# Performance work log

Measured on AMD Instinct MI355X. Metric: run time of the kernel, lower is better.

## Reference

```python
import jax, jax.numpy as jnp
import numpy as np
from jax import lax

B, T, N_OBS, N_ACT, H = 256, 4096, 64, 18, 8


def _linear_params(k, fan_out, fan_in):
    # torch nn.Linear default init: U(-1/sqrt(fan_in), 1/sqrt(fan_in))
    lim = 1.0 / np.sqrt(fan_in)
    kw, kb = jax.random.split(k)
    W = jax.random.uniform(kw, (fan_out, fan_in), minval=-lim, maxval=lim, dtype=jnp.float32)
    b = jax.random.uniform(kb, (fan_out,), minval=-lim, maxval=lim, dtype=jnp.float32)
    return W, b


def setup_inputs() -> dict:
    key = jax.random.key(0)
    ks = jax.random.split(key, 8)
    W1, b1 = _linear_params(ks[0], 4, N_OBS)          # linear1
    W2, b2 = _linear_params(ks[1], H, 4)              # linear2
    Wih, bih = _linear_params(ks[2], 4 * H, H)        # lstm input-hidden (i,f,g,o)
    Whh, bhh = _linear_params(ks[3], 4 * H, H)        # lstm hidden-hidden
    Wa, ba = _linear_params(ks[4], N_ACT, H)          # action_distribution
    Wv, bv = _linear_params(ks[5], 1, H)              # values
    states = jax.random.normal(ks[6], (B, T, N_OBS), dtype=jnp.float32)
    dones = jax.random.randint(ks[7], (B, T), 0, 2).astype(bool)
    hx = jnp.zeros((2, T, H), dtype=jnp.float32)
    return dict(states=states, dones=dones, hx=hx,
                W1=W1, b1=b1, W2=W2, b2=b2,
                Wih=Wih, bih=bih, Whh=Whh, bhh=bhh,
                Wa=Wa, ba=ba, Wv=Wv, bv=bv)


def reference(states, dones, hx, W1, b1, W2, b2, Wih, bih, Whh, bhh, Wa, ba, Wv, bv):
    b, t, _ = states.shape
    # MLP encoder on flattened [B*T, n_obs] (same math as original flatten)
    x = jax.nn.relu(jnp.einsum('btn,kn->btk', states, W1) + b1)   # [B,T,4]
    x = jax.nn.relu(jnp.einsum('btk,hk->bth', x, W2) + b2)        # [B,T,8]

    def step(carry, inp):
        h, c = carry                      # each [T,H] (lstm batch = trajectory_length)
        xt, dt = inp                      # [T,H], [T] bool
        mask = dt[:, None]                # done.view(1,-1,1) broadcast reset
        h = jnp.where(mask, 0.0, h)
        c = jnp.where(mask, 0.0, c)
        gates = xt @ Wih.T + bih + h @ Whh.T + bhh  # [T,4H]
        i, f, g, o = jnp.split(gates, 4, axis=-1)
        i = jax.nn.sigmoid(i)
        f = jax.nn.sigmoid(f)
        g = jnp.tanh(g)
        o = jax.nn.sigmoid(o)
        c2 = f * c + i * g
        h2 = o * jnp.tanh(c2)
        return (h2, c2), h2

    # sequential scan over the BATCH dim (faithful to the original unbind(dim=0) loop)
    _, lstm_out = lax.scan(step, (hx[0], hx[1]), (x, dones))      # [B,T,H]

    flat = lstm_out.reshape(b * t, -1)                            # cat(lstm_out, 0)
    actions = flat @ Wa.T + ba                                    # [B*T, n_actions]
    values = flat @ Wv.T + bv                                     # [B*T, 1]
    return actions.reshape(b, -1, t), values.reshape(b, t)
```

## Files before the change

kernel.cpp:

```cpp
#include <hip/hip_runtime.h>

#define T_DIM 4096
#define B_DIM 256
#define NSEG 8
#define SEGLEN 32
#define BSTRIDE ((size_t)T_DIM * 64)

#define SIGM(X)  __builtin_amdgcn_rcpf(1.f + __expf(-(X)))
#define TANH(X)  fmaf(2.f, __builtin_amdgcn_rcpf(1.f + __expf(-2.f * (X))), -1.f)


#define LOAD_WEIGHTS                                                           \
    float w1s[4][8];                                                           \
    _Pragma("unroll") for (int m = 0; m < 4; ++m)                              \
        _Pragma("unroll") for (int k = 0; k < 8; ++k)                          \
            w1s[m][k] = W1[m * 64 + j * 8 + k];                                \
    float b1r0 = b1[0], b1r1 = b1[1], b1r2 = b1[2], b1r3 = b1[3];              \
    float w2s0 = W2[j*4+0], w2s1 = W2[j*4+1], w2s2 = W2[j*4+2], w2s3 = W2[j*4+3]; \
    float b2r = b2[j];                                                         \
    float wI[8], wF[8], wG[8], wO[8], uI[8], uF[8], uG[8], uO[8];              \
    _Pragma("unroll") for (int k = 0; k < 8; ++k) {                            \
        wI[k] = Wih[j * 8 + k];        uI[k] = Whh[j * 8 + k];                 \
        wF[k] = Wih[(8 + j) * 8 + k];  uF[k] = Whh[(8 + j) * 8 + k];           \
        wG[k] = Wih[(16 + j) * 8 + k]; uG[k] = Whh[(16 + j) * 8 + k];          \
        wO[k] = Wih[(24 + j) * 8 + k]; uO[k] = Whh[(24 + j) * 8 + k];          \
    }                                                                          \
    float bI = bih[j] + bhh[j],      bF = bih[8 + j] + bhh[8 + j];             \
    float bG = bih[16 + j] + bhh[16 + j], bO = bih[24 + j] + bhh[24 + j];      \
    float hw0[8], hw1[8], hw2[8];                                              \
    float hb0 = ba[j], hb1 = ba[8 + j], hb2 = 0.f;                             \
    _Pragma("unroll") for (int k = 0; k < 8; ++k) {                            \
        hw0[k] = Wa[j * 8 + k]; hw1[k] = Wa[(8 + j) * 8 + k]; hw2[k] = 0.f;    \
    }                                                                          \
    if (j < 2) {                                                               \
        _Pragma("unroll") for (int k = 0; k < 8; ++k) hw2[k] = Wa[(16+j)*8+k]; \
        hb2 = ba[16 + j];                                                      \
    } else if (j == 2) {                                                       \
        _Pragma("unroll") for (int k = 0; k < 8; ++k) hw2[k] = Wv[k];          \
        hb2 = bv[0];                                                           \
    }

#define CORE_S(DONEE, SA, SV)                                                  \
        float p0 = SA.x * w1s[0][0], p1 = SA.x * w1s[1][0];                    \
        float p2 = SA.x * w1s[2][0], p3 = SA.x * w1s[3][0];                    \
        p0 = fmaf(SA.y, w1s[0][1], p0); p1 = fmaf(SA.y, w1s[1][1], p1);        \
        p2 = fmaf(SA.y, w1s[2][1], p2); p3 = fmaf(SA.y, w1s[3][1], p3);        \
        p0 = fmaf(SA.z, w1s[0][2], p0); p1 = fmaf(SA.z, w1s[1][2], p1);        \
        p2 = fmaf(SA.z, w1s[2][2], p2); p3 = fmaf(SA.z, w1s[3][2], p3);        \
        p0 = fmaf(SA.w, w1s[0][3], p0); p1 = fmaf(SA.w, w1s[1][3], p1);        \
        p2 = fmaf(SA.w, w1s[2][3], p2); p3 = fmaf(SA.w, w1s[3][3], p3);        \
        p0 = fmaf(SV.x, w1s[0][4], p0); p1 = fmaf(SV.x, w1s[1][4], p1);        \
        p2 = fmaf(SV.x, w1s[2][4], p2); p3 = fmaf(SV.x, w1s[3][4], p3);        \
        p0 = fmaf(SV.y, w1s[0][5], p0); p1 = fmaf(SV.y, w1s[1][5], p1);        \
        p2 = fmaf(SV.y, w1s[2][5], p2); p3 = fmaf(SV.y, w1s[3][5], p3);        \
        p0 = fmaf(SV.z, w1s[0][6], p0); p1 = fmaf(SV.z, w1s[1][6], p1);        \
        p2 = fmaf(SV.z, w1s[2][6], p2); p3 = fmaf(SV.z, w1s[3][6], p3);        \
        p0 = fmaf(SV.w, w1s[0][7], p0); p1 = fmaf(SV.w, w1s[1][7], p1);        \
        p2 = fmaf(SV.w, w1s[2][7], p2); p3 = fmaf(SV.w, w1s[3][7], p3);        \
        p0 += __shfl_xor(p0, 1, 64); p1 += __shfl_xor(p1, 1, 64);              \
        p2 += __shfl_xor(p2, 1, 64); p3 += __shfl_xor(p3, 1, 64);              \
        p0 += __shfl_xor(p0, 2, 64); p1 += __shfl_xor(p1, 2, 64);              \
        p2 += __shfl_xor(p2, 2, 64); p3 += __shfl_xor(p3, 2, 64);              \
        p0 += __shfl_xor(p0, 4, 64); p1 += __shfl_xor(p1, 4, 64);              \
        p2 += __shfl_xor(p2, 4, 64); p3 += __shfl_xor(p3, 4, 64);              \
        float y0 = fmaxf(p0 + b1r0, 0.f);                                      \
        float y1 = fmaxf(p1 + b1r1, 0.f);                                      \
        float y2 = fmaxf(p2 + b1r2, 0.f);                                      \
        float y3 = fmaxf(p3 + b1r3, 0.f);                                      \
        float xj = fmaf(y3, w2s3, fmaf(y2, w2s2, fmaf(y1, w2s1,                \
                   fmaf(y0, w2s0, b2r))));                                     \
        xj = fmaxf(xj, 0.f);                                                   \
        float x0 = __shfl(xj, gb | 0, 64);                                     \
        float x1 = __shfl(xj, gb | 1, 64);                                     \
        float xx2 = __shfl(xj, gb | 2, 64);                                    \
        float x3 = __shfl(xj, gb | 3, 64);                                     \
        float x4 = __shfl(xj, gb | 4, 64);                                     \
        float x5 = __shfl(xj, gb | 5, 64);                                     \
        float x6 = __shfl(xj, gb | 6, 64);                                     \
        float x7 = __shfl(xj, gb | 7, 64);                                     \
        float gi = bI, gf = bF, gg = bG, go = bO;                              \
        gi = fmaf(x0, wI[0], gi); gi = fmaf(x1, wI[1], gi);                    \
        gi = fmaf(xx2, wI[2], gi); gi = fmaf(x3, wI[3], gi);                   \
        gi = fmaf(x4, wI[4], gi); gi = fmaf(x5, wI[5], gi);                    \
        gi = fmaf(x6, wI[6], gi); gi = fmaf(x7, wI[7], gi);                    \
        gf = fmaf(x0, wF[0], gf); gf = fmaf(x1, wF[1], gf);                    \
        gf = fmaf(xx2, wF[2], gf); gf = fmaf(x3, wF[3], gf);                   \
        gf = fmaf(x4, wF[4], gf); gf = fmaf(x5, wF[5], gf);                    \
        gf = fmaf(x6, wF[6], gf); gf = fmaf(x7, wF[7], gf);                    \
        gg = fmaf(x0, wG[0], gg); gg = fmaf(x1, wG[1], gg);                    \
        gg = fmaf(xx2, wG[2], gg); gg = fmaf(x3, wG[3], gg);                   \
        gg = fmaf(x4, wG[4], gg); gg = fmaf(x5, wG[5], gg);                    \
        gg = fmaf(x6, wG[6], gg); gg = fmaf(x7, wG[7], gg);                    \
        go = fmaf(x0, wO[0], go); go = fmaf(x1, wO[1], go);                    \
        go = fmaf(xx2, wO[2], go); go = fmaf(x3, wO[3], go);                   \
        go = fmaf(x4, wO[4], go); go = fmaf(x5, wO[5], go);                    \
        go = fmaf(x6, wO[6], go); go = fmaf(x7, wO[7], go);                    \
        float dI = h[0] * uI[0], dF = h[0] * uF[0];                            \
        float dG = h[0] * uG[0], dO = h[0] * uO[0];                            \
        dI = fmaf(h[1], uI[1], dI); dF = fmaf(h[1], uF[1], dF);                \
        dG = fmaf(h[1], uG[1], dG); dO = fmaf(h[1], uO[1], dO);                \
        dI = fmaf(h[2], uI[2], dI); dF = fmaf(h[2], uF[2], dF);                \
        dG = fmaf(h[2], uG[2], dG); dO = fmaf(h[2], uO[2], dO);                \
        dI = fmaf(h[3], uI[3], dI); dF = fmaf(h[3], uF[3], dF);                \
        dG = fmaf(h[3], uG[3], dG); dO = fmaf(h[3], uO[3], dO);                \
        dI = fmaf(h[4], uI[4], dI); dF = fmaf(h[4], uF[4], dF);                \
        dG = fmaf(h[4], uG[4], dG); dO = fmaf(h[4], uO[4], dO);                \
        dI = fmaf(h[5], uI[5], dI); dF = fmaf(h[5], uF[5], dF);                \
        dG = fmaf(h[5], uG[5], dG); dO = fmaf(h[5], uO[5], dO);                \
        dI = fmaf(h[6], uI[6], dI); dF = fmaf(h[6], uF[6], dF);                \
        dG = fmaf(h[6], uG[6], dG); dO = fmaf(h[6], uO[6], dO);                \
        dI = fmaf(h[7], uI[7], dI); dF = fmaf(h[7], uF[7], dF);                \
        dG = fmaf(h[7], uG[7], dG); dO = fmaf(h[7], uO[7], dO);                \
        float GI = (DONEE) ? gi : (gi + dI);                                   \
        float GF = (DONEE) ? gf : (gf + dF);                                   \
        float GG = (DONEE) ? gg : (gg + dG);                                   \
        float GO = (DONEE) ? go : (go + dO);                                   \
        float cin = (DONEE) ? 0.f : c;                                         \
        float i_ = SIGM(GI);                                                   \
        float f_ = SIGM(GF);                                                   \
        float g_ = TANH(GG);                                                   \
        float o_ = SIGM(GO);                                                   \
        float c2 = fmaf(f_, cin, i_ * g_);                                     \
        float th = TANH(c2);                                                   \
        float h2 = o_ * th;

#define HEADS                                                                  \
        float o0 = hb0, o1 = hb1, o2 = hb2;                                    \
        o0 = fmaf(h[0], hw0[0], o0); o1 = fmaf(h[0], hw1[0], o1);              \
        o2 = fmaf(h[0], hw2[0], o2);                                           \
        o0 = fmaf(h[1], hw0[1], o0); o1 = fmaf(h[1], hw1[1], o1);              \
        o2 = fmaf(h[1], hw2[1], o2);                                           \
        o0 = fmaf(h[2], hw0[2], o0); o1 = fmaf(h[2], hw1[2], o1);              \
        o2 = fmaf(h[2], hw2[2], o2);                                           \
        o0 = fmaf(h[3], hw0[3], o0); o1 = fmaf(h[3], hw1[3], o1);              \
        o2 = fmaf(h[3], hw2[3], o2);                                           \
        o0 = fmaf(h[4], hw0[4], o0); o1 = fmaf(h[4], hw1[4], o1);              \
        o2 = fmaf(h[4], hw2[4], o2);                                           \
        o0 = fmaf(h[5], hw0[5], o0); o1 = fmaf(h[5], hw1[5], o1);              \
        o2 = fmaf(h[5], hw2[5], o2);                                           \
        o0 = fmaf(h[6], hw0[6], o0); o1 = fmaf(h[6], hw1[6], o1);              \
        o2 = fmaf(h[6], hw2[6], o2);                                           \
        o0 = fmaf(h[7], hw0[7], o0); o1 = fmaf(h[7], hw1[7], o1);              \
        o2 = fmaf(h[7], hw2[7], o2);

#define HSHFL                                                                  \
        h[0] = __shfl(h2, gb | 0, 64); h[1] = __shfl(h2, gb | 1, 64);          \
        h[2] = __shfl(h2, gb | 2, 64); h[3] = __shfl(h2, gb | 3, 64);          \
        h[4] = __shfl(h2, gb | 4, 64); h[5] = __shfl(h2, gb | 5, 64);          \
        h[6] = __shfl(h2, gb | 6, 64); h[7] = __shfl(h2, gb | 7, 64);

__global__ __launch_bounds__(64) void pass1_kernel(
    const float* __restrict__ states, const int* __restrict__ dones,
    const float* __restrict__ hx,
    const float* __restrict__ W1, const float* __restrict__ b1,
    const float* __restrict__ W2, const float* __restrict__ b2,
    const float* __restrict__ Wih, const float* __restrict__ bih,
    const float* __restrict__ Whh, const float* __restrict__ bhh,
    const float* __restrict__ Wa, const float* __restrict__ ba,
    const float* __restrict__ Wv, const float* __restrict__ bv,
    float* __restrict__ out,
    float* __restrict__ carryH, float* __restrict__ carryC,
    int* __restrict__ fdbuf)
{
    int lane = threadIdx.x;
    int col  = lane >> 3;
    int j    = lane & 7;
    int gb   = lane & 56;
    int s    = blockIdx.x >> 9;
    int tb   = blockIdx.x & 511;
    int t    = tb * 8 + col;
    int b0   = s * SEGLEN;

    LOAD_WEIGHTS

    float h[8]; float c;
    if (s == 0) {
#pragma unroll
        for (int m = 0; m < 8; ++m) h[m] = hx[t * 8 + m];
        c = hx[T_DIM * 8 + t * 8 + j];
    } else {
#pragma unroll
        for (int m = 0; m < 8; ++m) h[m] = 0.f;
        c = 0.f;
    }

    const float* sbase = states + ((size_t)b0 * T_DIM + t) * 64 + j * 8;
    const int*   dbase = dones + (size_t)b0 * T_DIM + t;
    float* outA = out + ((size_t)b0 * T_DIM + t) * 18;
    float* outV = out + (size_t)18 * B_DIM * T_DIM + (size_t)b0 * T_DIM + t;
    int fd = SEGLEN;

    int dn0, dn1, dn2, dn3;
    float4 sa0, sv0, sa1, sv1, sa2, sv2, sa3, sv3;
#define PF(I) \
    dn##I = dbase[(size_t)(I) * T_DIM]; \
    sa##I = *(const float4*)(sbase + (size_t)(I) * BSTRIDE); \
    sv##I = *(const float4*)(sbase + (size_t)(I) * BSTRIDE + 4);
    PF(0) PF(1) PF(2) PF(3)
#undef PF

#define P1STEP(KK, DN, SA, SV)                                                 \
    {                                                                          \
        int done = DN; float4 sa = SA, sv = SV;                                \
        int kp = (KK) + 4; kp = (kp > SEGLEN - 1) ? (SEGLEN - 1) : kp;         \
        DN = dbase[(size_t)kp * T_DIM];                                        \
        SA = *(const float4*)(sbase + (size_t)kp * BSTRIDE);                   \
        SV = *(const float4*)(sbase + (size_t)kp * BSTRIDE + 4);               \
        CORE_S(done, sa, sv)                                                   \
        c = c2;                                                                \
        HSHFL                                                                  \
        fd = (done && fd == SEGLEN) ? (KK) : fd;                               \
        HEADS                                                                  \
        outA[j] = o0; outA[8 + j] = o1;                                        \
        if (j < 2) outA[16 + j] = o2; else if (j == 2) *outV = o2;             \
        outA += (size_t)T_DIM * 18; outV += T_DIM;                             \
    }

    for (int k0 = 0; k0 < SEGLEN; k0 += 4) {
        P1STEP(k0 + 0, dn0, sa0, sv0);
        P1STEP(k0 + 1, dn1, sa1, sv1);
        P1STEP(k0 + 2, dn2, sa2, sv2);
        P1STEP(k0 + 3, dn3, sa3, sv3);
    }
#undef P1STEP

    carryH[((size_t)s * T_DIM + t) * 8 + j] = h[j];
    carryC[((size_t)s * T_DIM + t) * 8 + j] = c;
    if (j == 0) fdbuf[(size_t)s * T_DIM + t] = fd;
}

__global__ __launch_bounds__(64) void pass2_kernel(
    const float* __restrict__ states, const int* __restrict__ dones,
    const float* __restrict__ W1, const float* __restrict__ b1,
    const float* __restrict__ W2, const float* __restrict__ b2,
    const float* __restrict__ Wih, const float* __restrict__ bih,
    const float* __restrict__ Whh, const float* __restrict__ bhh,
    const float* __restrict__ Wa, const float* __restrict__ ba,
    const float* __restrict__ Wv, const float* __restrict__ bv,
    float* __restrict__ out,
    const float* __restrict__ carryH, const float* __restrict__ carryC,
    const int* __restrict__ fdbuf)
{
    int lane = threadIdx.x;
    int col  = lane >> 3;
    int j    = lane & 7;
    int gb   = lane & 56;
    int s    = 1 + (int)(blockIdx.x >> 9);
    int tb   = blockIdx.x & 511;
    int t    = tb * 8 + col;

    LOAD_WEIGHTS

    const float* sb2 = states + (size_t)t * 64 + j * 8;

    float h[8]; float c;
    bool prev_exact = (s == 1) ||
                      (fdbuf[(size_t)(s - 1) * T_DIM + t] < SEGLEN);
    if (__all(prev_exact)) {
#pragma unroll
        for (int m = 0; m < 8; ++m)
            h[m] = carryH[((size_t)(s - 1) * T_DIM + t) * 8 + m];
        c = carryC[((size_t)(s - 1) * T_DIM + t) * 8 + j];
    } else {
#pragma unroll
        for (int m = 0; m < 8; ++m) h[m] = carryH[(size_t)t * 8 + m];
        c = carryC[(size_t)t * 8 + j];
        for (int p = 1; p <= s - 1; ++p) {
            size_t bb = (size_t)p * SEGLEN;
            for (int k = 0; k < SEGLEN; ++k) {
                int done = dones[(bb + k) * T_DIM + t];
                float4 sa = *(const float4*)(sb2 + (bb + k) * BSTRIDE);
                float4 sv = *(const float4*)(sb2 + (bb + k) * BSTRIDE + 4);
                CORE_S(done, sa, sv)
                c = c2;
                HSHFL
            }
            int fdp = fdbuf[(size_t)p * T_DIM + t];
            if (fdp < SEGLEN) {
#pragma unroll
                for (int m = 0; m < 8; ++m)
                    h[m] = carryH[((size_t)p * T_DIM + t) * 8 + m];
                c = carryC[((size_t)p * T_DIM + t) * 8 + j];
            }
        }
    }

    int fd = fdbuf[(size_t)s * T_DIM + t];
    int wmax = fd;
#pragma unroll
    for (int d = 1; d < 64; d <<= 1) {
        int o = __shfl_xor(wmax, d, 64);
        wmax = (o > wmax) ? o : wmax;
    }
    size_t bbase = (size_t)s * SEGLEN;
    float4 csa = *(const float4*)(sb2 + bbase * BSTRIDE);
    float4 csv = *(const float4*)(sb2 + bbase * BSTRIDE + 4);
    for (int k = 0; k < wmax; ++k) {
        bool act = (k < fd);
        float4 sa = csa, sv = csv;
        int kn = k + 1; kn = (kn > SEGLEN - 1) ? (SEGLEN - 1) : kn;
        csa = *(const float4*)(sb2 + (bbase + kn) * BSTRIDE);
        csv = *(const float4*)(sb2 + (bbase + kn) * BSTRIDE + 4);
        CORE_S(0, sa, sv)
        c = act ? c2 : c;
        float n0 = __shfl(h2, gb | 0, 64), n1 = __shfl(h2, gb | 1, 64);
        float n2 = __shfl(h2, gb | 2, 64), n3 = __shfl(h2, gb | 3, 64);
        float n4 = __shfl(h2, gb | 4, 64), n5 = __shfl(h2, gb | 5, 64);
        float n6 = __shfl(h2, gb | 6, 64), n7 = __shfl(h2, gb | 7, 64);
        h[0] = act ? n0 : h[0]; h[1] = act ? n1 : h[1];
        h[2] = act ? n2 : h[2]; h[3] = act ? n3 : h[3];
        h[4] = act ? n4 : h[4]; h[5] = act ? n5 : h[5];
        h[6] = act ? n6 : h[6]; h[7] = act ? n7 : h[7];
        HEADS
        if (act) {
            float* outA = out + ((bbase + k) * T_DIM + t) * 18;
            outA[j] = o0; outA[8 + j] = o1;
            if (j < 2) outA[16 + j] = o2;
            else if (j == 2)
                out[(size_t)18 * B_DIM * T_DIM + (bbase + k) * T_DIM + t] = o2;
        }
    }
}

extern "C" void kernel_launch(void* const* d_in, const int* in_sizes, int n_in,
                              void* d_out, int out_size, void* d_ws, size_t ws_size,
                              hipStream_t stream) {
    (void)in_sizes; (void)n_in; (void)out_size; (void)ws_size;
    const float* states = (const float*)d_in[0];
    const int*   dones  = (const int*)d_in[1];
    const float* hx     = (const float*)d_in[2];
    const float* W1     = (const float*)d_in[3];
    const float* b1     = (const float*)d_in[4];
    const float* W2     = (const float*)d_in[5];
    const float* b2     = (const float*)d_in[6];
    const float* Wih    = (const float*)d_in[7];
    const float* bih    = (const float*)d_in[8];
    const float* Whh    = (const float*)d_in[9];
    const float* bhh    = (const float*)d_in[10];
    const float* Wa     = (const float*)d_in[11];
    const float* ba     = (const float*)d_in[12];
    const float* Wv     = (const float*)d_in[13];
    const float* bv     = (const float*)d_in[14];
    float* out = (float*)d_out;

    float* carryH = (float*)d_ws;
    float* carryC = (float*)((char*)d_ws + (1u << 20));
    int*   fdbuf  = (int*)((char*)d_ws + (2u << 20));

    pass1_kernel<<<NSEG * 512, 64, 0, stream>>>(states, dones, hx, W1, b1, W2, b2,
                                                Wih, bih, Whh, bhh, Wa, ba, Wv, bv,
                                                out, carryH, carryC, fdbuf);
    pass2_kernel<<<(NSEG - 1) * 512, 64, 0, stream>>>(states, dones, W1, b1, W2, b2,
                                                      Wih, bih, Whh, bhh, Wa, ba, Wv, bv,
                                                      out, carryH, carryC, fdbuf);
}
```

Baseline: 96.17 us.

## Replace lane shuffles with DPP xor-gathers and compute layer-2 redundantly per lane

The 8-lane hidden-state broadcast now uses an xor-permuted layout, built from DPP quad_perm moves for xor 1 and 2 and ds_bpermute only for xor 4. To match, the Whh, head and initial-state weights are reindexed by j^m. The first two reduction stages also switch to DPP. Each lane now computes all eight layer-2 outputs itself instead of shuffling them, and the pass1 prefetch depth drops from 4 to 2. The aim is to cut LDS-permute latency on the serial recurrence, in exchange for extra FMAs, more registers and a shallower load prefetch.

```diff
diff --git a/kernel.cpp b/kernel.cpp
--- a/kernel.cpp
+++ b/kernel.cpp
@@ -8,6 +8,15 @@
 
 #define SIGM(X)  __builtin_amdgcn_rcpf(1.f + __expf(-(X)))
 #define TANH(X)  fmaf(2.f, __builtin_amdgcn_rcpf(1.f + __expf(-2.f * (X))), -1.f)
+
+__device__ __forceinline__ float dpp_xor1(float x) {
+    return __int_as_float(__builtin_amdgcn_update_dpp(
+        0, __float_as_int(x), 0xB1, 0xF, 0xF, true));
+}
+__device__ __forceinline__ float dpp_xor2(float x) {
+    return __int_as_float(__builtin_amdgcn_update_dpp(
+        0, __float_as_int(x), 0x4E, 0xF, 0xF, true));
+}
 
 
 #define LOAD_WEIGHTS                                                           \
@@ -16,27 +25,39 @@
         _Pragma("unroll") for (int k = 0; k < 8; ++k)                          \
             w1s[m][k] = W1[m * 64 + j * 8 + k];                                \
     float b1r0 = b1[0], b1r1 = b1[1], b1r2 = b1[2], b1r3 = b1[3];              \
-    float w2s0 = W2[j*4+0], w2s1 = W2[j*4+1], w2s2 = W2[j*4+2], w2s3 = W2[j*4+3]; \
-    float b2r = b2[j];                                                         \
+    float w2a[8][4]; float b2a[8];                                             \
+    _Pragma("unroll") for (int m = 0; m < 8; ++m) {                            \
+        b2a[m] = b2[m];                                                        \
+        _Pragma("unroll") for (int k = 0; k < 4; ++k)                          \
+            w2a[m][k] = W2[m * 4 + k];                                         \
+    }                                                                          \
     float wI[8], wF[8], wG[8], wO[8], uI[8], uF[8], uG[8], uO[8];              \
     _Pragma("unroll") for (int k = 0; k < 8; ++k) {                            \
-        wI[k] = Wih[j * 8 + k];        uI[k] = Whh[j * 8 + k];                 \
-        wF[k] = Wih[(8 + j) * 8 + k];  uF[k] = Whh[(8 + j) * 8 + k];           \
-        wG[k] = Wih[(16 + j) * 8 + k]; uG[k] = Whh[(16 + j) * 8 + k];          \
-        wO[k] = Wih[(24 + j) * 8 + k]; uO[k] = Whh[(24 + j) * 8 + k];          \
+        wI[k] = Wih[j * 8 + k];                                                \
+        wF[k] = Wih[(8 + j) * 8 + k];                                          \
+        wG[k] = Wih[(16 + j) * 8 + k];                                         \
+        wO[k] = Wih[(24 + j) * 8 + k];                                         \
+    }                                                                          \
+    _Pragma("unroll") for (int m = 0; m < 8; ++m) {                            \
+        int kk = j ^ m;                                                        \
+        uI[m] = Whh[j * 8 + kk];                                               \
+        uF[m] = Whh[(8 + j) * 8 + kk];                                         \
+        uG[m] = Whh[(16 + j) * 8 + kk];                                        \
+        uO[m] = Whh[(24 + j) * 8 + kk];                                        \
     }                                                                          \
     float bI = bih[j] + bhh[j],      bF = bih[8 + j] + bhh[8 + j];             \
     float bG = bih[16 + j] + bhh[16 + j], bO = bih[24 + j] + bhh[24 + j];      \
     float hw0[8], hw1[8], hw2[8];                                              \
     float hb0 = ba[j], hb1 = ba[8 + j], hb2 = 0.f;                             \
-    _Pragma("unroll") for (int k = 0; k < 8; ++k) {                            \
-        hw0[k] = Wa[j * 8 + k]; hw1[k] = Wa[(8 + j) * 8 + k]; hw2[k] = 0.f;    \
+    _Pragma("unroll") for (int m = 0; m < 8; ++m) {                            \
+        int kk = j ^ m;                                                        \
+        hw0[m] = Wa[j * 8 + kk]; hw1[m] = Wa[(8 + j) * 8 + kk]; hw2[m] = 0.f;  \
     }                                                                          \
     if (j < 2) {                                                               \
-        _Pragma("unroll") for (int k = 0; k < 8; ++k) hw2[k] = Wa[(16+j)*8+k]; \
+        _Pragma("unroll") for (int m = 0; m < 8; ++m) hw2[m] = Wa[(16+j)*8+(j^m)]; \
         hb2 = ba[16 + j];                                                      \
     } else if (j == 2) {                                                       \
-        _Pragma("unroll") for (int k = 0; k < 8; ++k) hw2[k] = Wv[k];          \
+        _Pragma("unroll") for (int m = 0; m < 8; ++m) hw2[m] = Wv[j ^ m];      \
         hb2 = bv[0];                                                           \
     }
 
@@ -57,27 +78,32 @@
         p2 = fmaf(SV.z, w1s[2][6], p2); p3 = fmaf(SV.z, w1s[3][6], p3);        \
         p0 = fmaf(SV.w, w1s[0][7], p0); p1 = fmaf(SV.w, w1s[1][7], p1);        \
         p2 = fmaf(SV.w, w1s[2][7], p2); p3 = fmaf(SV.w, w1s[3][7], p3);        \
-        p0 += __shfl_xor(p0, 1, 64); p1 += __shfl_xor(p1, 1, 64);              \
-        p2 += __shfl_xor(p2, 1, 64); p3 += __shfl_xor(p3, 1, 64);              \
-        p0 += __shfl_xor(p0, 2, 64); p1 += __shfl_xor(p1, 2, 64);              \
-        p2 += __shfl_xor(p2, 2, 64); p3 += __shfl_xor(p3, 2, 64);              \
+        p0 += dpp_xor1(p0); p1 += dpp_xor1(p1);                                \
+        p2 += dpp_xor1(p2); p3 += dpp_xor1(p3);                                \
+        p0 += dpp_xor2(p0); p1 += dpp_xor2(p1);                                \
+        p2 += dpp_xor2(p2); p3 += dpp_xor2(p3);                                \
         p0 += __shfl_xor(p0, 4, 64); p1 += __shfl_xor(p1, 4, 64);              \
         p2 += __shfl_xor(p2, 4, 64); p3 += __shfl_xor(p3, 4, 64);              \
         float y0 = fmaxf(p0 + b1r0, 0.f);                                      \
         float y1 = fmaxf(p1 + b1r1, 0.f);                                      \
         float y2 = fmaxf(p2 + b1r2, 0.f);                                      \
         float y3 = fmaxf(p3 + b1r3, 0.f);                                      \
-        float xj = fmaf(y3, w2s3, fmaf(y2, w2s2, fmaf(y1, w2s1,                \
-                   fmaf(y0, w2s0, b2r))));                                     \
-        xj = fmaxf(xj, 0.f);                                                   \
-        float x0 = __shfl(xj, gb | 0, 64);                                     \
-        float x1 = __shfl(xj, gb | 1, 64);                                     \
-        float xx2 = __shfl(xj, gb | 2, 64);                                    \
-        float x3 = __shfl(xj, gb | 3, 64);                                     \
-        float x4 = __shfl(xj, gb | 4, 64);                                     \
-        float x5 = __shfl(xj, gb | 5, 64);                                     \
-        float x6 = __shfl(xj, gb | 6, 64);                                     \
-        float x7 = __shfl(xj, gb | 7, 64);                                     \
+        float x0 = fmaxf(fmaf(y3, w2a[0][3], fmaf(y2, w2a[0][2],               \
+                   fmaf(y1, w2a[0][1], fmaf(y0, w2a[0][0], b2a[0])))), 0.f);   \
+        float x1 = fmaxf(fmaf(y3, w2a[1][3], fmaf(y2, w2a[1][2],               \
+                   fmaf(y1, w2a[1][1], fmaf(y0, w2a[1][0], b2a[1])))), 0.f);   \
+        float xx2 = fmaxf(fmaf(y3, w2a[2][3], fmaf(y2, w2a[2][2],              \
+                   fmaf(y1, w2a[2][1], fmaf(y0, w2a[2][0], b2a[2])))), 0.f);   \
+        float x3 = fmaxf(fmaf(y3, w2a[3][3], fmaf(y2, w2a[3][2],               \
+                   fmaf(y1, w2a[3][1], fmaf(y0, w2a[3][0], b2a[3])))), 0.f);   \
+        float x4 = fmaxf(fmaf(y3, w2a[4][3], fmaf(y2, w2a[4][2],               \
+                   fmaf(y1, w2a[4][1], fmaf(y0, w2a[4][0], b2a[4])))), 0.f);   \
+        float x5 = fmaxf(fmaf(y3, w2a[5][3], fmaf(y2, w2a[5][2],               \
+                   fmaf(y1, w2a[5][1], fmaf(y0, w2a[5][0], b2a[5])))), 0.f);   \
+        float x6 = fmaxf(fmaf(y3, w2a[6][3], fmaf(y2, w2a[6][2],               \
+                   fmaf(y1, w2a[6][1], fmaf(y0, w2a[6][0], b2a[6])))), 0.f);   \
+        float x7 = fmaxf(fmaf(y3, w2a[7][3], fmaf(y2, w2a[7][2],               \
+                   fmaf(y1, w2a[7][1], fmaf(y0, w2a[7][0], b2a[7])))), 0.f);   \
         float gi = bI, gf = bF, gg = bG, go = bO;                              \
         gi = fmaf(x0, wI[0], gi); gi = fmaf(x1, wI[1], gi);                    \
         gi = fmaf(xx2, wI[2], gi); gi = fmaf(x3, wI[3], gi);                   \
@@ -124,6 +150,16 @@
         float th = TANH(c2);                                                   \
         float h2 = o_ * th;
 
+#define HGATHER(DST, SRC)                                                      \
+        DST[0] = SRC;                                                          \
+        DST[1] = dpp_xor1(DST[0]);                                             \
+        DST[2] = dpp_xor2(DST[0]);                                             \
+        DST[3] = dpp_xor2(DST[1]);                                             \
+        DST[4] = __shfl_xor(DST[0], 4, 64);                                    \
+        DST[5] = __shfl_xor(DST[1], 4, 64);                                    \
+        DST[6] = __shfl_xor(DST[2], 4, 64);                                    \
+        DST[7] = __shfl_xor(DST[3], 4, 64);
+
 #define HEADS                                                                  \
         float o0 = hb0, o1 = hb1, o2 = hb2;                                    \
         o0 = fmaf(h[0], hw0[0], o0); o1 = fmaf(h[0], hw1[0], o1);              \
@@ -143,12 +179,6 @@
         o0 = fmaf(h[7], hw0[7], o0); o1 = fmaf(h[7], hw1[7], o1);              \
         o2 = fmaf(h[7], hw2[7], o2);
 
-#define HSHFL                                                                  \
-        h[0] = __shfl(h2, gb | 0, 64); h[1] = __shfl(h2, gb | 1, 64);          \
-        h[2] = __shfl(h2, gb | 2, 64); h[3] = __shfl(h2, gb | 3, 64);          \
-        h[4] = __shfl(h2, gb | 4, 64); h[5] = __shfl(h2, gb | 5, 64);          \
-        h[6] = __shfl(h2, gb | 6, 64); h[7] = __shfl(h2, gb | 7, 64);
-
 __global__ __launch_bounds__(64) void pass1_kernel(
     const float* __restrict__ states, const int* __restrict__ dones,
     const float* __restrict__ hx,
@@ -165,7 +195,6 @@
     int lane = threadIdx.x;
     int col  = lane >> 3;
     int j    = lane & 7;
-    int gb   = lane & 56;
     int s    = blockIdx.x >> 9;
     int tb   = blockIdx.x & 511;
     int t    = tb * 8 + col;
@@ -176,7 +205,7 @@
     float h[8]; float c;
     if (s == 0) {
 #pragma unroll
-        for (int m = 0; m < 8; ++m) h[m] = hx[t * 8 + m];
+        for (int m = 0; m < 8; ++m) h[m] = hx[t * 8 + (j ^ m)];
         c = hx[T_DIM * 8 + t * 8 + j];
     } else {
 #pragma unroll
@@ -190,25 +219,25 @@
     float* outV = out + (size_t)18 * B_DIM * T_DIM + (size_t)b0 * T_DIM + t;
     int fd = SEGLEN;
 
-    int dn0, dn1, dn2, dn3;
-    float4 sa0, sv0, sa1, sv1, sa2, sv2, sa3, sv3;
+    int dn0, dn1;
+    float4 sa0, sv0, sa1, sv1;
 #define PF(I) \
     dn##I = dbase[(size_t)(I) * T_DIM]; \
     sa##I = *(const float4*)(sbase + (size_t)(I) * BSTRIDE); \
     sv##I = *(const float4*)(sbase + (size_t)(I) * BSTRIDE + 4);
-    PF(0) PF(1) PF(2) PF(3)
+    PF(0) PF(1)
 #undef PF
 
 #define P1STEP(KK, DN, SA, SV)                                                 \
     {                                                                          \
         int done = DN; float4 sa = SA, sv = SV;                                \
-        int kp = (KK) + 4; kp = (kp > SEGLEN - 1) ? (SEGLEN - 1) : kp;         \
+        int kp = (KK) + 2; kp = (kp > SEGLEN - 1) ? (SEGLEN - 1) : kp;         \
         DN = dbase[(size_t)kp * T_DIM];                                        \
         SA = *(const float4*)(sbase + (size_t)kp * BSTRIDE);                   \
         SV = *(const float4*)(sbase + (size_t)kp * BSTRIDE + 4);               \
         CORE_S(done, sa, sv)                                                   \
         c = c2;                                                                \
-        HSHFL                                                                  \
+        HGATHER(h, h2)                                                         \
         fd = (done && fd == SEGLEN) ? (KK) : fd;                               \
         HEADS                                                                  \
         outA[j] = o0; outA[8 + j] = o1;                                        \
@@ -216,15 +245,13 @@
         outA += (size_t)T_DIM * 18; outV += T_DIM;                             \
     }
 
-    for (int k0 = 0; k0 < SEGLEN; k0 += 4) {
+    for (int k0 = 0; k0 < SEGLEN; k0 += 2) {
         P1STEP(k0 + 0, dn0, sa0, sv0);
         P1STEP(k0 + 1, dn1, sa1, sv1);
-        P1STEP(k0 + 2, dn2, sa2, sv2);
-        P1STEP(k0 + 3, dn3, sa3, sv3);
     }
 #undef P1STEP
 
-    carryH[((size_t)s * T_DIM + t) * 8 + j] = h[j];
+    carryH[((size_t)s * T_DIM + t) * 8 + j] = h[0];
     carryC[((size_t)s * T_DIM + t) * 8 + j] = c;
     if (j == 0) fdbuf[(size_t)s * T_DIM + t] = fd;
 }
@@ -244,7 +271,6 @@
     int lane = threadIdx.x;
     int col  = lane >> 3;
     int j    = lane & 7;
-    int gb   = lane & 56;
     int s    = 1 + (int)(blockIdx.x >> 9);
     int tb   = blockIdx.x & 511;
     int t    = tb * 8 + col;
@@ -259,11 +285,11 @@
     if (__all(prev_exact)) {
 #pragma unroll
         for (int m = 0; m < 8; ++m)
-            h[m] = carryH[((size_t)(s - 1) * T_DIM + t) * 8 + m];
+            h[m] = carryH[((size_t)(s - 1) * T_DIM + t) * 8 + (j ^ m)];
         c = carryC[((size_t)(s - 1) * T_DIM + t) * 8 + j];
     } else {
 #pragma unroll
-        for (int m = 0; m < 8; ++m) h[m] = carryH[(size_t)t * 8 + m];
+        for (int m = 0; m < 8; ++m) h[m] = carryH[(size_t)t * 8 + (j ^ m)];
         c = carryC[(size_t)t * 8 + j];
         for (int p = 1; p <= s - 1; ++p) {
             size_t bb = (size_t)p * SEGLEN;
@@ -273,13 +299,13 @@
                 float4 sv = *(const float4*)(sb2 + (bb + k) * BSTRIDE + 4);
                 CORE_S(done, sa, sv)
                 c = c2;
-                HSHFL
+                HGATHER(h, h2)
             }
             int fdp = fdbuf[(size_t)p * T_DIM + t];
             if (fdp < SEGLEN) {
 #pragma unroll
                 for (int m = 0; m < 8; ++m)
-                    h[m] = carryH[((size_t)p * T_DIM + t) * 8 + m];
+                    h[m] = carryH[((size_t)p * T_DIM + t) * 8 + (j ^ m)];
                 c = carryC[((size_t)p * T_DIM + t) * 8 + j];
             }
         }
@@ -303,14 +329,10 @@
         csv = *(const float4*)(sb2 + (bbase + kn) * BSTRIDE + 4);
         CORE_S(0, sa, sv)
         c = act ? c2 : c;
-        float n0 = __shfl(h2, gb | 0, 64), n1 = __shfl(h2, gb | 1, 64);
-        float n2 = __shfl(h2, gb | 2, 64), n3 = __shfl(h2, gb | 3, 64);
-        float n4 = __shfl(h2, gb | 4, 64), n5 = __shfl(h2, gb | 5, 64);
-        float n6 = __shfl(h2, gb | 6, 64), n7 = __shfl(h2, gb | 7, 64);
-        h[0] = act ? n0 : h[0]; h[1] = act ? n1 : h[1];
-        h[2] = act ? n2 : h[2]; h[3] = act ? n3 : h[3];
-        h[4] = act ? n4 : h[4]; h[5] = act ? n5 : h[5];
-        h[6] = act ? n6 : h[6]; h[7] = act ? n7 : h[7];
+        float hn[8];
+        HGATHER(hn, h2)
+#pragma unroll
+        for (int m = 0; m < 8; ++m) h[m] = act ? hn[m] : h[m];
         HEADS
         if (act) {
             float* outA = out + ((bbase + k) * T_DIM + t) * 18;
```

New measurement: 105.1 us. +9.3%, slower.
